# Kernel tuning notes

Hardware: AMD Instinct MI355X
Metric: run time of the kernel (lower is better)

Reference implementation:

```python
import jax, jax.numpy as jnp
import numpy as np

D = 256        # n_unit
H = 2          # n_head
FF = 256       # n_hid
WIN = 99       # N-1 in source: row i attends to cols [i-99, i]
NEG = -1e30    # additive mask value (-inf in torch)
LN_EPS = 1e-5


def _layer_norm(x, w, b):
    mu = jnp.mean(x, axis=-1, keepdims=True)
    var = jnp.mean((x - mu) ** 2, axis=-1, keepdims=True)
    return (x - mu) * jax.lax.rsqrt(var + LN_EPS) * w + b


def _pos_encoding(S, d):
    pos = jnp.arange(S, dtype=jnp.float32)[:, None]                      # [S,1]
    div = jnp.exp(jnp.arange(0, d, 2, dtype=jnp.float32) * (-np.log(10000.0) / d))
    ang = pos * div                                                      # [S,d/2]
    return jnp.stack([jnp.sin(ang), jnp.cos(ang)], axis=-1).reshape(S, d)


def _band_mask(S):
    i = jnp.arange(S)[:, None]
    j = jnp.arange(S)[None, :]
    allowed = (j <= i) & (j >= i - WIN)
    return jnp.where(allowed, 0.0, NEG).astype(jnp.float32)             # [S,S]


def setup_inputs() -> dict:
    key = jax.random.key(0)
    ks = jax.random.split(key, 24)
    B, S, IN = 8, 2000, 256
    s = 0.02
    inp = {
        "src": jax.random.normal(ks[0], (B, S, IN), jnp.float32),
        "input_lengths": jax.random.randint(ks[1], (B,), 1, S + 1).astype(jnp.int64),
        # encoder Linear(in_size, n_unit); torch Linear weight is [out,in]
        "W_enc": jax.random.normal(ks[2], (D, IN), jnp.float32) * s,
        "b_enc": jnp.zeros((D,), jnp.float32),
        # MHA packed qkv projection
        "in_proj_w": jax.random.normal(ks[3], (3 * D, D), jnp.float32) * s,
        "in_proj_b": jnp.zeros((3 * D,), jnp.float32),
        "out_proj_w": jax.random.normal(ks[4], (D, D), jnp.float32) * s,
        "out_proj_b": jnp.zeros((D,), jnp.float32),
        "ln1_w": jnp.ones((D,), jnp.float32),
        "ln1_b": jnp.zeros((D,), jnp.float32),
        # FFN
        "lin1_w": jax.random.normal(ks[5], (FF, D), jnp.float32) * s,
        "lin1_b": jnp.zeros((FF,), jnp.float32),
        "lin2_w": jax.random.normal(ks[6], (D, FF), jnp.float32) * s,
        "lin2_b": jnp.zeros((D,), jnp.float32),
        "ln2_w": jnp.ones((D,), jnp.float32),
        "ln2_b": jnp.zeros((D,), jnp.float32),
        # output head
        "fc1_w": jax.random.normal(ks[7], (D // 4, D), jnp.float32) * s,
        "fc1_b": jnp.zeros((D // 4,), jnp.float32),
        "fc2_w": jax.random.normal(ks[8], (1, D // 4), jnp.float32) * s,
        "fc2_b": jnp.zeros((1,), jnp.float32),
    }
    return inp


def reference(src, input_lengths, W_enc, b_enc, in_proj_w, in_proj_b,
              out_proj_w, out_proj_b, ln1_w, ln1_b, lin1_w, lin1_b,
              lin2_w, lin2_b, ln2_w, ln2_b, fc1_w, fc1_b, fc2_w, fc2_b):
    B, S, _ = src.shape
    hd = D // H
    # input projection + positional encoding (dropout is identity at eval)
    x = src @ W_enc.T + b_enc                                            # [B,S,D]
    x = x + _pos_encoding(S, D)[None]
    # --- TransformerEncoderLayer (post-norm, relu) with banded causal mask ---
    qkv = x @ in_proj_w.T + in_proj_b                                    # [B,S,3D]
    q, k, v = jnp.split(qkv, 3, axis=-1)
    q = q.reshape(B, S, H, hd)
    k = k.reshape(B, S, H, hd)
    v = v.reshape(B, S, H, hd)
    scores = jnp.einsum('bihd,bjhd->bhij', q, k) / np.sqrt(hd)           # [B,H,S,S]
    scores = scores + _band_mask(S)[None, None]
    attn = jax.nn.softmax(scores, axis=-1)
    ctx = jnp.einsum('bhij,bjhd->bihd', attn, v).reshape(B, S, D)
    attn_out = ctx @ out_proj_w.T + out_proj_b
    x = _layer_norm(x + attn_out, ln1_w, ln1_b)
    ff = jax.nn.relu(x @ lin1_w.T + lin1_b) @ lin2_w.T + lin2_b
    x = _layer_norm(x + ff, ln2_w, ln2_b)
    # --- output head (no activation between fc1 and fc2, per source) ---
    out = x @ fc1_w.T + fc1_b                                            # [B,S,D/4]
    logits = out @ fc2_w.T + fc2_b                                       # [B,S,1]
    return logits.reshape(B, -1)                                         # [B,S]
```

## Files before the change

### kernel.cpp

```cpp
#include <hip/hip_runtime.h>
#include <math.h>

#define SLEN 2000
#define BATCH 8
#define MTOK 16000
#define WIN 99
#define XPAD 264

typedef __attribute__((ext_vector_type(8))) short short8;
typedef __attribute__((ext_vector_type(4))) float floatx4;

__device__ __forceinline__ float bf2f(unsigned int h) {
  union { unsigned int u; float f; } w; w.u = h << 16; return w.f;
}
__device__ __forceinline__ unsigned short f2bf(float f) {
  union { float f; unsigned int u; } w; w.f = f;
  return (unsigned short)((w.u + 0x7fffu + ((w.u >> 16) & 1u)) >> 16);
}

__device__ __forceinline__ void cvt4(const float* __restrict__ in,
                                     unsigned short* __restrict__ out, int i) {
  float4 v = ((const float4*)in)[i];
  ushort4 o;
  o.x = f2bf(v.x); o.y = f2bf(v.y); o.z = f2bf(v.z); o.w = f2bf(v.w);
  ((ushort4*)out)[i] = o;
}

__global__ __launch_bounds__(256) void k_prep(
    const float* __restrict__ wenc,     unsigned short* __restrict__ wencb,
    const float* __restrict__ wqk,      unsigned short* __restrict__ wqkb,
    const float* __restrict__ wout,     unsigned short* __restrict__ woutb,
    const float* __restrict__ wl1,      unsigned short* __restrict__ wl1b,
    const float* __restrict__ wl2,      unsigned short* __restrict__ wl2b,
    float* __restrict__ pe,
    const float* __restrict__ fc1w, const float* __restrict__ fc1b,
    const float* __restrict__ fc2w, const float* __restrict__ fc2b,
    const float* __restrict__ ln2w, const float* __restrict__ ln2b,
    float* __restrict__ hp) {
  __shared__ float red0[4], red1[4];
  const int bx = blockIdx.x, tid = threadIdx.x;
  if (bx < 64)         { cvt4(wenc, wencb, bx * 256 + tid); }
  else if (bx < 256)   { cvt4(wqk,  wqkb,  (bx - 64) * 256 + tid); }
  else if (bx < 320)   { cvt4(wout, woutb, (bx - 256) * 256 + tid); }
  else if (bx < 384)   { cvt4(wl1,  wl1b,  (bx - 320) * 256 + tid); }
  else if (bx < 448)   { cvt4(wl2,  wl2b,  (bx - 384) * 256 + tid); }
  else if (bx < 948) {
    int i4 = (bx - 448) * 256 + tid;
    int e0 = i4 * 4;
    int s  = e0 >> 8;
    int d0 = e0 & 255;
    float dv0 = expf((float)(d0 >> 1) * -0.07195578415606394f);
    float dv1 = expf((float)((d0 >> 1) + 1) * -0.07195578415606394f);
    float a0 = (float)s * dv0, a1 = (float)s * dv1;
    ((float4*)pe)[i4] = make_float4(sinf(a0), cosf(a0), sinf(a1), cosf(a1));
  } else {
    int k = tid;
    float we = 0.f;
#pragma unroll 8
    for (int o = 0; o < 64; ++o) we += fc2w[o] * fc1w[o * 256 + k];
    float c1 = ln2w[k] * we;
    hp[k] = c1;
    float p0 = ln2b[k] * we;
    if (k < 64) p0 += fc2w[k] * fc1b[k];
    float s0 = p0, s1 = c1;
#pragma unroll
    for (int off = 32; off; off >>= 1) {
      s0 += __shfl_xor(s0, off);
      s1 += __shfl_xor(s1, off);
    }
    int wv = k >> 6;
    if ((k & 63) == 0) { red0[wv] = s0; red1[wv] = s1; }
    __syncthreads();
    if (k == 0) {
      hp[256] = red0[0] + red0[1] + red0[2] + red0[3] + fc2b[0];
      hp[257] = red1[0] + red1[1] + red1[2] + red1[3];
    }
  }
}

__global__ __launch_bounds__(512) void k_pre(
    const float* __restrict__ src,
    const unsigned short* __restrict__ wenc, const float* __restrict__ benc,
    const float* __restrict__ pe,
    const unsigned short* __restrict__ wqk, const float* __restrict__ bqk,
    unsigned short* __restrict__ xb, unsigned short* __restrict__ qkvb) {
  __shared__ __align__(16) unsigned short Xt[64 * XPAD];
  const int tid = threadIdx.x, lane = tid & 63, w = tid >> 6;
  const int m0 = blockIdx.x * 64;
  const int kq = lane >> 4, ml = lane & 15;

  {
    const int cb = w * 32;
    floatx4 acc[4][2] = {};
#pragma unroll
    for (int k8 = 0; k8 < 8; ++k8) {
      const int kt = k8 * 32;
      short8 af[4];
#pragma unroll
      for (int mt = 0; mt < 4; ++mt) {
        const float* ap = src + (size_t)(m0 + mt * 16 + ml) * 256 + kt + kq * 8;
        float4 v0 = *(const float4*)ap;
        float4 v1 = *(const float4*)(ap + 4);
        unsigned short t8[8] = {f2bf(v0.x), f2bf(v0.y), f2bf(v0.z), f2bf(v0.w),
                                f2bf(v1.x), f2bf(v1.y), f2bf(v1.z), f2bf(v1.w)};
        af[mt] = *(const short8*)t8;
      }
#pragma unroll
      for (int nt = 0; nt < 2; ++nt) {
        short8 bf = *(const short8*)(wenc + (size_t)(cb + nt * 16 + ml) * 256 + kt + kq * 8);
#pragma unroll
        for (int mt = 0; mt < 4; ++mt)
          acc[mt][nt] = __builtin_amdgcn_mfma_f32_16x16x32_bf16(af[mt], bf, acc[mt][nt], 0, 0, 0);
      }
    }
#pragma unroll
    for (int mt = 0; mt < 4; ++mt)
#pragma unroll
      for (int nt = 0; nt < 2; ++nt)
#pragma unroll
        for (int r = 0; r < 4; ++r) {
          int lrow = mt * 16 + kq * 4 + r;
          int col  = cb + nt * 16 + ml;
          float v = acc[mt][nt][r] + benc[col]
                  + pe[(size_t)((m0 + lrow) % SLEN) * 256 + col];
          unsigned short hv = f2bf(v);
          Xt[lrow * XPAD + col] = hv;
          xb[(size_t)(m0 + lrow) * 256 + col] = hv;
        }
  }
  __syncthreads();

  {
    const int cb = w * 96;
    floatx4 acc[4][6] = {};
#pragma unroll
    for (int k8 = 0; k8 < 8; ++k8) {
      const int kt = k8 * 32;
      short8 af[4];
#pragma unroll
      for (int mt = 0; mt < 4; ++mt)
        af[mt] = *(const short8*)&Xt[(mt * 16 + ml) * XPAD + kt + kq * 8];
#pragma unroll
      for (int nt = 0; nt < 6; ++nt) {
        short8 bf = *(const short8*)(wqk + (size_t)(cb + nt * 16 + ml) * 256 + kt + kq * 8);
#pragma unroll
        for (int mt = 0; mt < 4; ++mt)
          acc[mt][nt] = __builtin_amdgcn_mfma_f32_16x16x32_bf16(af[mt], bf, acc[mt][nt], 0, 0, 0);
      }
    }
#pragma unroll
    for (int mt = 0; mt < 4; ++mt)
#pragma unroll
      for (int nt = 0; nt < 6; ++nt)
#pragma unroll
        for (int r = 0; r < 4; ++r) {
          int row = m0 + mt * 16 + kq * 4 + r;
          int cg  = cb + nt * 16 + ml;
          qkvb[(size_t)row * 768 + cg] = f2bf(acc[mt][nt][r] + bqk[cg]);
        }
  }
}

#define KPAD 136
#define VPAD 184
#define PPAD 132
#define UNION 176

__global__ __launch_bounds__(256) void k_attn_mfma(const unsigned short* __restrict__ qkv,
                                                   unsigned short* __restrict__ ctx) {
  __shared__ __align__(16) unsigned short KV[UNION * KPAD];
  __shared__ __align__(16) unsigned short Ps[4][16 * PPAD];
  const int tid  = threadIdx.x;
  const int lane = tid & 63;
  const int w    = tid >> 6;
  const int i0   = blockIdx.x * 64;
  const int b    = blockIdx.y;
  const int h    = blockIdx.z;
  const int jmin_u = i0 - WIN;
  const float scale = 0.08838834764831845f;

  const int qrow = i0 + w * 16 + (lane & 15);
  const unsigned short* qptr =
      qkv + (size_t)(b * SLEN + min(qrow, SLEN - 1)) * 768 + h * 128 + (lane >> 4) * 8;
  short8 qf[4];
#pragma unroll
  for (int kc = 0; kc < 4; ++kc) qf[kc] = *(const short8*)(qptr + kc * 32);

  for (int it = 0; it < 11; ++it) {
    int idx = it * 256 + tid;
    int row = idx >> 4;
    int c8  = idx & 15;
    int j = jmin_u + row;
    uint4 v = make_uint4(0u, 0u, 0u, 0u);
    if (j >= 0 && j < SLEN)
      v = *(const uint4*)(qkv + (size_t)(b * SLEN + j) * 768 + 256 + h * 128 + c8 * 8);
    *(uint4*)&KV[row * KPAD + c8 * 8] = v;
  }
  __syncthreads();

  const int koff = w * 16;
  floatx4 sc[8] = {};
#pragma unroll
  for (int kt = 0; kt < 8; ++kt) {
#pragma unroll
    for (int kc = 0; kc < 4; ++kc) {
      short8 kf = *(const short8*)&KV[(koff + kt * 16 + (lane & 15)) * KPAD
                                      + kc * 32 + (lane >> 4) * 8];
      sc[kt] = __builtin_amdgcn_mfma_f32_16x16x32_bf16(qf[kc], kf, sc[kt], 0, 0, 0);
    }
  }

  const int qme = i0 + w * 16 + (lane >> 4) * 4;
  const int jme = jmin_u + koff + (lane & 15);
  float mx[4] = {-1e30f, -1e30f, -1e30f, -1e30f};
#pragma unroll
  for (int kt = 0; kt < 8; ++kt) {
#pragma unroll
    for (int r = 0; r < 4; ++r) {
      int j = jme + kt * 16, q = qme + r;
      bool ok = (j >= 0) && (j >= q - WIN) && (j <= q);
      float s = ok ? sc[kt][r] : -1e30f;
      sc[kt][r] = s;
      mx[r] = fmaxf(mx[r], s);
    }
  }
#pragma unroll
  for (int r = 0; r < 4; ++r)
#pragma unroll
    for (int off = 8; off; off >>= 1) mx[r] = fmaxf(mx[r], __shfl_xor(mx[r], off, 16));

  float sum[4] = {0.f, 0.f, 0.f, 0.f};
#pragma unroll
  for (int kt = 0; kt < 8; ++kt)
#pragma unroll
    for (int r = 0; r < 4; ++r) {
      float e = __expf((sc[kt][r] - mx[r]) * scale);
      sc[kt][r] = e;
      sum[r] += e;
    }
#pragma unroll
  for (int r = 0; r < 4; ++r)
#pragma unroll
    for (int off = 8; off; off >>= 1) sum[r] += __shfl_xor(sum[r], off, 16);
  float rinv[4];
#pragma unroll
  for (int r = 0; r < 4; ++r) rinv[r] = 1.f / sum[r];

  unsigned short* pw = &Ps[w][0];
#pragma unroll
  for (int kt = 0; kt < 8; ++kt)
#pragma unroll
    for (int r = 0; r < 4; ++r)
      pw[((lane >> 4) * 4 + r) * PPAD + kt * 16 + (lane & 15)] = f2bf(sc[kt][r]);
  __syncthreads();

  for (int it = 0; it < 12; ++it) {
    int idx = it * 256 + tid;
    int grp = idx >> 6;
    int key = (grp >> 4) * 64 + (idx & 63);
    int c8  = grp & 15;
    if (key < UNION) {
      int j = jmin_u + key;
      uint4 v = make_uint4(0u, 0u, 0u, 0u);
      if (j >= 0 && j < SLEN)
        v = *(const uint4*)(qkv + (size_t)(b * SLEN + j) * 768 + 512 + h * 128 + c8 * 8);
      unsigned short e[8];
      *(uint4*)e = v;
      int d0 = c8 * 8;
#pragma unroll
      for (int i = 0; i < 8; ++i) KV[(d0 + i) * VPAD + key] = e[i];
    }
  }
  __syncthreads();

  floatx4 ov[8] = {};
#pragma unroll
  for (int kc = 0; kc < 4; ++kc) {
    short8 pf = *(const short8*)&pw[(lane & 15) * PPAD + kc * 32 + (lane >> 4) * 8];
#pragma unroll
    for (int dt = 0; dt < 8; ++dt) {
      short8 vf = *(const short8*)&KV[(dt * 16 + (lane & 15)) * VPAD
                                      + koff + kc * 32 + (lane >> 4) * 8];
      ov[dt] = __builtin_amdgcn_mfma_f32_16x16x32_bf16(pf, vf, ov[dt], 0, 0, 0);
    }
  }

#pragma unroll
  for (int dt = 0; dt < 8; ++dt)
#pragma unroll
    for (int r = 0; r < 4; ++r) {
      int q = qme + r;
      if (q < SLEN)
        ctx[(size_t)(b * SLEN + q) * 256 + h * 128 + dt * 16 + (lane & 15)] =
            f2bf(ov[dt][r] * rinv[r]);
    }
}

__global__ __launch_bounds__(512) void k_post(
    const unsigned short* __restrict__ ctx,
    const unsigned short* __restrict__ wout, const float* __restrict__ bout,
    const unsigned short* __restrict__ xb,
    const float* __restrict__ ln1w, const float* __restrict__ ln1b,
    const unsigned short* __restrict__ w1, const float* __restrict__ b1,
    const unsigned short* __restrict__ w2, const float* __restrict__ b2,
    const float* __restrict__ hp, float* __restrict__ out) {
  __shared__ __align__(16) unsigned short X1[64 * XPAD];
  __shared__ float lnred[8][64][3];
  __shared__ float lnstat[64][2];
  __shared__ float lnp[512];
  __shared__ float c1s[256];
  const int tid = threadIdx.x, lane = tid & 63, w = tid >> 6;
  const int m0 = blockIdx.x * 64;
  const int kq = lane >> 4, ml = lane & 15;
  const int cb = w * 32;

  if (tid < 256) {
    lnp[tid] = ln1w[tid];
    lnp[256 + tid] = ln1b[tid];
    c1s[tid] = hp[tid];
  }
  const float c0h = hp[256], sc1 = hp[257];

  floatx4 acc[4][2] = {};
#pragma unroll
  for (int k8 = 0; k8 < 8; ++k8) {
    const int kt = k8 * 32;
    short8 af[4];
#pragma unroll
    for (int mt = 0; mt < 4; ++mt)
      af[mt] = *(const short8*)(ctx + (size_t)(m0 + mt * 16 + ml) * 256 + kt + kq * 8);
#pragma unroll
    for (int nt = 0; nt < 2; ++nt) {
      short8 bf = *(const short8*)(wout + (size_t)(cb + nt * 16 + ml) * 256 + kt + kq * 8);
#pragma unroll
      for (int mt = 0; mt < 4; ++mt)
        acc[mt][nt] = __builtin_amdgcn_mfma_f32_16x16x32_bf16(af[mt], bf, acc[mt][nt], 0, 0, 0);
    }
  }
  float s_[4][4], q_[4][4];
#pragma unroll
  for (int mt = 0; mt < 4; ++mt)
#pragma unroll
    for (int r = 0; r < 4; ++r) { s_[mt][r] = 0.f; q_[mt][r] = 0.f; }
#pragma unroll
  for (int mt = 0; mt < 4; ++mt)
#pragma unroll
    for (int nt = 0; nt < 2; ++nt)
#pragma unroll
      for (int r = 0; r < 4; ++r) {
        int lrow = mt * 16 + kq * 4 + r;
        int col  = cb + nt * 16 + ml;
        float v = acc[mt][nt][r] + bout[col]
                + bf2f(xb[(size_t)(m0 + lrow) * 256 + col]);
        acc[mt][nt][r] = v;
        s_[mt][r] += v;
        q_[mt][r] += v * v;
      }
#pragma unroll
  for (int mt = 0; mt < 4; ++mt)
#pragma unroll
    for (int r = 0; r < 4; ++r) {
#pragma unroll
      for (int off = 8; off; off >>= 1) {
        s_[mt][r] += __shfl_xor(s_[mt][r], off, 16);
        q_[mt][r] += __shfl_xor(q_[mt][r], off, 16);
      }
      if (ml == 0) {
        int lrow = mt * 16 + kq * 4 + r;
        lnred[w][lrow][0] = s_[mt][r];
        lnred[w][lrow][1] = q_[mt][r];
      }
    }
  __syncthreads();
  if (tid < 64) {
    float s = 0.f, q = 0.f;
#pragma unroll
    for (int i = 0; i < 8; ++i) { s += lnred[i][tid][0]; q += lnred[i][tid][1]; }
    float mu  = s * (1.f / 256.f);
    float var = q * (1.f / 256.f) - mu * mu;
    lnstat[tid][0] = mu;
    lnstat[tid][1] = rsqrtf(var + 1e-5f);
  }
  __syncthreads();
  floatx4 x1sav[4][2];
#pragma unroll
  for (int mt = 0; mt < 4; ++mt)
#pragma unroll
    for (int r = 0; r < 4; ++r) {
      int lrow = mt * 16 + kq * 4 + r;
      float mu = lnstat[lrow][0], rr = lnstat[lrow][1];
#pragma unroll
      for (int nt = 0; nt < 2; ++nt) {
        int col = cb + nt * 16 + ml;
        float x1 = (acc[mt][nt][r] - mu) * rr * lnp[col] + lnp[256 + col];
        x1sav[mt][nt][r] = x1;
        X1[lrow * XPAD + col] = f2bf(x1);
      }
    }
  __syncthreads();

#pragma unroll
  for (int mt = 0; mt < 4; ++mt)
#pragma unroll
    for (int nt = 0; nt < 2; ++nt) acc[mt][nt] = (floatx4){0.f, 0.f, 0.f, 0.f};
#pragma unroll
  for (int k8 = 0; k8 < 8; ++k8) {
    const int kt = k8 * 32;
    short8 af[4];
#pragma unroll
    for (int mt = 0; mt < 4; ++mt)
      af[mt] = *(const short8*)&X1[(mt * 16 + ml) * XPAD + kt + kq * 8];
#pragma unroll
    for (int nt = 0; nt < 2; ++nt) {
      short8 bf = *(const short8*)(w1 + (size_t)(cb + nt * 16 + ml) * 256 + kt + kq * 8);
#pragma unroll
      for (int mt = 0; mt < 4; ++mt)
        acc[mt][nt] = __builtin_amdgcn_mfma_f32_16x16x32_bf16(af[mt], bf, acc[mt][nt], 0, 0, 0);
    }
  }
  __syncthreads();
#pragma unroll
  for (int mt = 0; mt < 4; ++mt)
#pragma unroll
    for (int nt = 0; nt < 2; ++nt)
#pragma unroll
      for (int r = 0; r < 4; ++r) {
        int lrow = mt * 16 + kq * 4 + r;
        int col  = cb + nt * 16 + ml;
        X1[lrow * XPAD + col] = f2bf(fmaxf(acc[mt][nt][r] + b1[col], 0.f));
      }
  __syncthreads();

#pragma unroll
  for (int mt = 0; mt < 4; ++mt)
#pragma unroll
    for (int nt = 0; nt < 2; ++nt) acc[mt][nt] = (floatx4){0.f, 0.f, 0.f, 0.f};
#pragma unroll
  for (int k8 = 0; k8 < 8; ++k8) {
    const int kt = k8 * 32;
    short8 af[4];
#pragma unroll
    for (int mt = 0; mt < 4; ++mt)
      af[mt] = *(const short8*)&X1[(mt * 16 + ml) * XPAD + kt + kq * 8];
#pragma unroll
    for (int nt = 0; nt < 2; ++nt) {
      short8 bf = *(const short8*)(w2 + (size_t)(cb + nt * 16 + ml) * 256 + kt + kq * 8);
#pragma unroll
      for (int mt = 0; mt < 4; ++mt)
        acc[mt][nt] = __builtin_amdgcn_mfma_f32_16x16x32_bf16(af[mt], bf, acc[mt][nt], 0, 0, 0);
    }
  }
  float ss[4][4], qq[4][4], dd[4][4];
#pragma unroll
  for (int mt = 0; mt < 4; ++mt)
#pragma unroll
    for (int r = 0; r < 4; ++r) { ss[mt][r] = 0.f; qq[mt][r] = 0.f; dd[mt][r] = 0.f; }
#pragma unroll
  for (int mt = 0; mt < 4; ++mt)
#pragma unroll
    for (int nt = 0; nt < 2; ++nt)
#pragma unroll
      for (int r = 0; r < 4; ++r) {
        int col = cb + nt * 16 + ml;
        float v = acc[mt][nt][r] + b2[col] + x1sav[mt][nt][r];
        ss[mt][r] += v;
        qq[mt][r] += v * v;
        dd[mt][r] += v * c1s[col];
      }
#pragma unroll
  for (int mt = 0; mt < 4; ++mt)
#pragma unroll
    for (int r = 0; r < 4; ++r) {
#pragma unroll
      for (int off = 8; off; off >>= 1) {
        ss[mt][r] += __shfl_xor(ss[mt][r], off, 16);
        qq[mt][r] += __shfl_xor(qq[mt][r], off, 16);
        dd[mt][r] += __shfl_xor(dd[mt][r], off, 16);
      }
      if (ml == 0) {
        int lrow = mt * 16 + kq * 4 + r;
        lnred[w][lrow][0] = ss[mt][r];
        lnred[w][lrow][1] = qq[mt][r];
        lnred[w][lrow][2] = dd[mt][r];
      }
    }
  __syncthreads();
  if (tid < 64) {
    float s = 0.f, q = 0.f, d = 0.f;
#pragma unroll
    for (int i = 0; i < 8; ++i) {
      s += lnred[i][tid][0];
      q += lnred[i][tid][1];
      d += lnred[i][tid][2];
    }
    float mu  = s * (1.f / 256.f);
    float var = q * (1.f / 256.f) - mu * mu;
    float rr  = rsqrtf(var + 1e-5f);
    out[m0 + tid] = rr * (d - mu * sc1) + c0h;
  }
}

extern "C" void kernel_launch(void* const* d_in, const int* in_sizes, int n_in,
                              void* d_out, int out_size, void* d_ws, size_t ws_size,
                              hipStream_t stream) {
  const float* src        = (const float*)d_in[0];
  const float* W_enc      = (const float*)d_in[2];
  const float* b_enc      = (const float*)d_in[3];
  const float* in_proj_w  = (const float*)d_in[4];
  const float* in_proj_b  = (const float*)d_in[5];
  const float* out_proj_w = (const float*)d_in[6];
  const float* out_proj_b = (const float*)d_in[7];
  const float* ln1_w      = (const float*)d_in[8];
  const float* ln1_b      = (const float*)d_in[9];
  const float* lin1_w     = (const float*)d_in[10];
  const float* lin1_b     = (const float*)d_in[11];
  const float* lin2_w     = (const float*)d_in[12];
  const float* lin2_b     = (const float*)d_in[13];
  const float* ln2_w      = (const float*)d_in[14];
  const float* ln2_b      = (const float*)d_in[15];
  const float* fc1_w      = (const float*)d_in[16];
  const float* fc1_b      = (const float*)d_in[17];
  const float* fc2_w      = (const float*)d_in[18];
  const float* fc2_b      = (const float*)d_in[19];

  char* p = (char*)d_ws;
  float* pe            = (float*)p;           p += (size_t)SLEN * 256 * 4;
  float* hp            = (float*)p;           p += 2048;
  unsigned short* xb   = (unsigned short*)p;  p += (size_t)MTOK * 256 * 2;
  unsigned short* qkvb = (unsigned short*)p;  p += (size_t)MTOK * 768 * 2;
  unsigned short* ctxb = (unsigned short*)p;  p += (size_t)MTOK * 256 * 2;
  unsigned short* wencb= (unsigned short*)p;  p += 256 * 256 * 2;
  unsigned short* wqkb = (unsigned short*)p;  p += 768 * 256 * 2;
  unsigned short* woutb= (unsigned short*)p;  p += 256 * 256 * 2;
  unsigned short* wl1b = (unsigned short*)p;  p += 256 * 256 * 2;
  unsigned short* wl2b = (unsigned short*)p;  p += 256 * 256 * 2;

  k_prep<<<949, 256, 0, stream>>>(W_enc, wencb, in_proj_w, wqkb,
                                  out_proj_w, woutb, lin1_w, wl1b, lin2_w, wl2b,
                                  pe, fc1_w, fc1_b, fc2_w, fc2_b, ln2_w, ln2_b, hp);
  k_pre<<<MTOK / 64, 512, 0, stream>>>(src, wencb, b_enc, pe, wqkb, in_proj_b, xb, qkvb);
  k_attn_mfma<<<dim3((SLEN + 63) / 64, BATCH, 2), 256, 0, stream>>>(qkvb, ctxb);
  k_post<<<MTOK / 64, 512, 0, stream>>>(ctxb, woutb, out_proj_b, xb, ln1_w, ln1_b,
                                        wl1b, lin1_b, wl2b, lin2_b, hp, (float*)d_out);
}
```

Baseline: 188.8 us.

## Split fused pre/post kernels into smaller kernels with more blocks

Splits the fused encoder+QKV kernel into separate k_enc and k_qkv launches, each with a 2D grid over column tiles. Splits the post kernel into an out-projection+LN1 kernel and an FFN+LN2+head kernel over 32-row tiles. The aim is more blocks and higher occupancy through smaller register and shared-memory footprints. In exchange it adds extra launches and round-trips of intermediate activations (xb, x1b) through global memory, and k_enc recomputes the src bf16 conversion for each column tile.

Result: slower. 218.3 us (+15.6%).

```diff
diff --git a/kernel.cpp b/kernel.cpp
--- a/kernel.cpp
+++ b/kernel.cpp
@@ -78,87 +78,85 @@
   }
 }
 
-__global__ __launch_bounds__(512) void k_pre(
+__global__ __launch_bounds__(256, 4) void k_enc(
     const float* __restrict__ src,
     const unsigned short* __restrict__ wenc, const float* __restrict__ benc,
-    const float* __restrict__ pe,
-    const unsigned short* __restrict__ wqk, const float* __restrict__ bqk,
-    unsigned short* __restrict__ xb, unsigned short* __restrict__ qkvb) {
-  __shared__ __align__(16) unsigned short Xt[64 * XPAD];
+    const float* __restrict__ pe, unsigned short* __restrict__ xb) {
   const int tid = threadIdx.x, lane = tid & 63, w = tid >> 6;
   const int m0 = blockIdx.x * 64;
+  const int cb = blockIdx.y * 128 + w * 32;
   const int kq = lane >> 4, ml = lane & 15;
 
-  {
-    const int cb = w * 32;
-    floatx4 acc[4][2] = {};
-#pragma unroll
-    for (int k8 = 0; k8 < 8; ++k8) {
-      const int kt = k8 * 32;
-      short8 af[4];
-#pragma unroll
-      for (int mt = 0; mt < 4; ++mt) {
-        const float* ap = src + (size_t)(m0 + mt * 16 + ml) * 256 + kt + kq * 8;
-        float4 v0 = *(const float4*)ap;
-        float4 v1 = *(const float4*)(ap + 4);
-        unsigned short t8[8] = {f2bf(v0.x), f2bf(v0.y), f2bf(v0.z), f2bf(v0.w),
-                                f2bf(v1.x), f2bf(v1.y), f2bf(v1.z), f2bf(v1.w)};
-        af[mt] = *(const short8*)t8;
-      }
-#pragma unroll
-      for (int nt = 0; nt < 2; ++nt) {
-        short8 bf = *(const short8*)(wenc + (size_t)(cb + nt * 16 + ml) * 256 + kt + kq * 8);
-#pragma unroll
-        for (int mt = 0; mt < 4; ++mt)
-          acc[mt][nt] = __builtin_amdgcn_mfma_f32_16x16x32_bf16(af[mt], bf, acc[mt][nt], 0, 0, 0);
-      }
-    }
+  floatx4 acc[4][2] = {};
+#pragma unroll
+  for (int k8 = 0; k8 < 8; ++k8) {
+    const int kt = k8 * 32;
+    short8 af[4];
+#pragma unroll
+    for (int mt = 0; mt < 4; ++mt) {
+      const float* ap = src + (size_t)(m0 + mt * 16 + ml) * 256 + kt + kq * 8;
+      float4 v0 = *(const float4*)ap;
+      float4 v1 = *(const float4*)(ap + 4);
+      unsigned short t8[8] = {f2bf(v0.x), f2bf(v0.y), f2bf(v0.z), f2bf(v0.w),
+                              f2bf(v1.x), f2bf(v1.y), f2bf(v1.z), f2bf(v1.w)};
+      af[mt] = *(const short8*)t8;
+    }
+#pragma unroll
+    for (int nt = 0; nt < 2; ++nt) {
+      short8 bf = *(const short8*)(wenc + (size_t)(cb + nt * 16 + ml) * 256 + kt + kq * 8);
+#pragma unroll
+      for (int mt = 0; mt < 4; ++mt)
+        acc[mt][nt] = __builtin_amdgcn_mfma_f32_16x16x32_bf16(af[mt], bf, acc[mt][nt], 0, 0, 0);
+    }
+  }
+#pragma unroll
+  for (int mt = 0; mt < 4; ++mt)
+#pragma unroll
+    for (int nt = 0; nt < 2; ++nt)
+#pragma unroll
+      for (int r = 0; r < 4; ++r) {
+        int m   = m0 + mt * 16 + kq * 4 + r;
+        int col = cb + nt * 16 + ml;
+        float v = acc[mt][nt][r] + benc[col] + pe[(size_t)(m % SLEN) * 256 + col];
+        xb[(size_t)m * 256 + col] = f2bf(v);
+      }
+}
+
+__global__ __launch_bounds__(256, 4) void k_qkv(
+    const unsigned short* __restrict__ xb,
+    const unsigned short* __restrict__ wqk, const float* __restrict__ bqk,
+    unsigned short* __restrict__ qkvb) {
+  const int tid = threadIdx.x, lane = tid & 63, w = tid >> 6;
+  const int m0 = blockIdx.x * 64;
+  const int cb = blockIdx.y * 128 + w * 32;
+  const int kq = lane >> 4, ml = lane & 15;
+
+  floatx4 acc[4][2] = {};
+#pragma unroll
+  for (int k8 = 0; k8 < 8; ++k8) {
+    const int kt = k8 * 32;
+    short8 af[4];
 #pragma unroll
     for (int mt = 0; mt < 4; ++mt)
-#pragma unroll
-      for (int nt = 0; nt < 2; ++nt)
-#pragma unroll
-        for (int r = 0; r < 4; ++r) {
-          int lrow = mt * 16 + kq * 4 + r;
-          int col  = cb + nt * 16 + ml;
-          float v = acc[mt][nt][r] + benc[col]
-                  + pe[(size_t)((m0 + lrow) % SLEN) * 256 + col];
-          unsigned short hv = f2bf(v);
-          Xt[lrow * XPAD + col] = hv;
-          xb[(size_t)(m0 + lrow) * 256 + col] = hv;
-        }
-  }
-  __syncthreads();
-
-  {
-    const int cb = w * 96;
-    floatx4 acc[4][6] = {};
-#pragma unroll
-    for (int k8 = 0; k8 < 8; ++k8) {
-      const int kt = k8 * 32;
-      short8 af[4];
+      af[mt] = *(const short8*)(xb + (size_t)(m0 + mt * 16 + ml) * 256 + kt + kq * 8);
+#pragma unroll
+    for (int nt = 0; nt < 2; ++nt) {
+      short8 bf = *(const short8*)(wqk + (size_t)(cb + nt * 16 + ml) * 256 + kt + kq * 8);
 #pragma unroll
       for (int mt = 0; mt < 4; ++mt)
-        af[mt] = *(const short8*)&Xt[(mt * 16 + ml) * XPAD + kt + kq * 8];
-#pragma unroll
-      for (int nt = 0; nt < 6; ++nt) {
-        short8 bf = *(const short8*)(wqk + (size_t)(cb + nt * 16 + ml) * 256 + kt + kq * 8);
-#pragma unroll
-        for (int mt = 0; mt < 4; ++mt)
-          acc[mt][nt] = __builtin_amdgcn_mfma_f32_16x16x32_bf16(af[mt], bf, acc[mt][nt], 0, 0, 0);
-      }
-    }
-#pragma unroll
-    for (int mt = 0; mt < 4; ++mt)
-#pragma unroll
-      for (int nt = 0; nt < 6; ++nt)
-#pragma unroll
-        for (int r = 0; r < 4; ++r) {
-          int row = m0 + mt * 16 + kq * 4 + r;
-          int cg  = cb + nt * 16 + ml;
-          qkvb[(size_t)row * 768 + cg] = f2bf(acc[mt][nt][r] + bqk[cg]);
-        }
-  }
+        acc[mt][nt] = __builtin_amdgcn_mfma_f32_16x16x32_bf16(af[mt], bf, acc[mt][nt], 0, 0, 0);
+    }
+  }
+#pragma unroll
+  for (int mt = 0; mt < 4; ++mt)
+#pragma unroll
+    for (int nt = 0; nt < 2; ++nt)
+#pragma unroll
+      for (int r = 0; r < 4; ++r) {
+        int m   = m0 + mt * 16 + kq * 4 + r;
+        int col = cb + nt * 16 + ml;
+        qkvb[(size_t)m * 768 + col] = f2bf(acc[mt][nt][r] + bqk[col]);
+      }
 }
 
 #define KPAD 136
@@ -296,56 +294,48 @@
     }
 }
 
-__global__ __launch_bounds__(512) void k_post(
+__global__ __launch_bounds__(256, 4) void k_o(
     const unsigned short* __restrict__ ctx,
     const unsigned short* __restrict__ wout, const float* __restrict__ bout,
     const unsigned short* __restrict__ xb,
     const float* __restrict__ ln1w, const float* __restrict__ ln1b,
-    const unsigned short* __restrict__ w1, const float* __restrict__ b1,
-    const unsigned short* __restrict__ w2, const float* __restrict__ b2,
-    const float* __restrict__ hp, float* __restrict__ out) {
-  __shared__ __align__(16) unsigned short X1[64 * XPAD];
-  __shared__ float lnred[8][64][3];
-  __shared__ float lnstat[64][2];
+    unsigned short* __restrict__ x1b) {
+  __shared__ float lnred[4][32][2];
+  __shared__ float lnstat[32][2];
   __shared__ float lnp[512];
-  __shared__ float c1s[256];
   const int tid = threadIdx.x, lane = tid & 63, w = tid >> 6;
-  const int m0 = blockIdx.x * 64;
+  const int m0 = blockIdx.x * 32;
+  const int cb = w * 64;
   const int kq = lane >> 4, ml = lane & 15;
-  const int cb = w * 32;
-
-  if (tid < 256) {
-    lnp[tid] = ln1w[tid];
-    lnp[256 + tid] = ln1b[tid];
-    c1s[tid] = hp[tid];
-  }
-  const float c0h = hp[256], sc1 = hp[257];
-
-  floatx4 acc[4][2] = {};
+
+  lnp[tid] = ln1w[tid];
+  lnp[256 + tid] = ln1b[tid];
+
+  floatx4 acc[2][4] = {};
 #pragma unroll
   for (int k8 = 0; k8 < 8; ++k8) {
     const int kt = k8 * 32;
-    short8 af[4];
-#pragma unroll
-    for (int mt = 0; mt < 4; ++mt)
+    short8 af[2];
+#pragma unroll
+    for (int mt = 0; mt < 2; ++mt)
       af[mt] = *(const short8*)(ctx + (size_t)(m0 + mt * 16 + ml) * 256 + kt + kq * 8);
 #pragma unroll
-    for (int nt = 0; nt < 2; ++nt) {
+    for (int nt = 0; nt < 4; ++nt) {
       short8 bf = *(const short8*)(wout + (size_t)(cb + nt * 16 + ml) * 256 + kt + kq * 8);
 #pragma unroll
-      for (int mt = 0; mt < 4; ++mt)
+      for (int mt = 0; mt < 2; ++mt)
         acc[mt][nt] = __builtin_amdgcn_mfma_f32_16x16x32_bf16(af[mt], bf, acc[mt][nt], 0, 0, 0);
     }
   }
-  float s_[4][4], q_[4][4];
-#pragma unroll
-  for (int mt = 0; mt < 4; ++mt)
+  float s_[2][4], q_[2][4];
+#pragma unroll
+  for (int mt = 0; mt < 2; ++mt)
 #pragma unroll
     for (int r = 0; r < 4; ++r) { s_[mt][r] = 0.f; q_[mt][r] = 0.f; }
 #pragma unroll
-  for (int mt = 0; mt < 4; ++mt)
-#pragma unroll
-    for (int nt = 0; nt < 2; ++nt)
+  for (int mt = 0; mt < 2; ++mt)
+#pragma unroll
+    for (int nt = 0; nt < 4; ++nt)
 #pragma unroll
       for (int r = 0; r < 4; ++r) {
         int lrow = mt * 16 + kq * 4 + r;
@@ -357,7 +347,7 @@
         q_[mt][r] += v * v;
       }
 #pragma unroll
-  for (int mt = 0; mt < 4; ++mt)
+  for (int mt = 0; mt < 2; ++mt)
 #pragma unroll
     for (int r = 0; r < 4; ++r) {
 #pragma unroll
@@ -372,103 +362,114 @@
       }
     }
   __syncthreads();
-  if (tid < 64) {
-    float s = 0.f, q = 0.f;
-#pragma unroll
-    for (int i = 0; i < 8; ++i) { s += lnred[i][tid][0]; q += lnred[i][tid][1]; }
+  if (tid < 32) {
+    float s = lnred[0][tid][0] + lnred[1][tid][0] + lnred[2][tid][0] + lnred[3][tid][0];
+    float q = lnred[0][tid][1] + lnred[1][tid][1] + lnred[2][tid][1] + lnred[3][tid][1];
     float mu  = s * (1.f / 256.f);
     float var = q * (1.f / 256.f) - mu * mu;
     lnstat[tid][0] = mu;
     lnstat[tid][1] = rsqrtf(var + 1e-5f);
   }
   __syncthreads();
-  floatx4 x1sav[4][2];
-#pragma unroll
-  for (int mt = 0; mt < 4; ++mt)
+#pragma unroll
+  for (int mt = 0; mt < 2; ++mt)
 #pragma unroll
     for (int r = 0; r < 4; ++r) {
       int lrow = mt * 16 + kq * 4 + r;
       float mu = lnstat[lrow][0], rr = lnstat[lrow][1];
 #pragma unroll
-      for (int nt = 0; nt < 2; ++nt) {
+      for (int nt = 0; nt < 4; ++nt) {
         int col = cb + nt * 16 + ml;
         float x1 = (acc[mt][nt][r] - mu) * rr * lnp[col] + lnp[256 + col];
-        x1sav[mt][nt][r] = x1;
-        X1[lrow * XPAD + col] = f2bf(x1);
-      }
-    }
-  __syncthreads();
-
-#pragma unroll
-  for (int mt = 0; mt < 4; ++mt)
-#pragma unroll
-    for (int nt = 0; nt < 2; ++nt) acc[mt][nt] = (floatx4){0.f, 0.f, 0.f, 0.f};
+        x1b[(size_t)(m0 + lrow) * 256 + col] = f2bf(x1);
+      }
+    }
+}
+
+__global__ __launch_bounds__(256, 4) void k_ffn(
+    const unsigned short* __restrict__ x1b,
+    const unsigned short* __restrict__ w1, const float* __restrict__ b1,
+    const unsigned short* __restrict__ w2, const float* __restrict__ b2,
+    const float* __restrict__ hp, float* __restrict__ out) {
+  __shared__ __align__(16) unsigned short Hs[32 * XPAD];
+  __shared__ float lnred[4][32][3];
+  __shared__ float c1s[256];
+  const int tid = threadIdx.x, lane = tid & 63, w = tid >> 6;
+  const int m0 = blockIdx.x * 32;
+  const int cb = w * 64;
+  const int kq = lane >> 4, ml = lane & 15;
+
+  c1s[tid] = hp[tid];
+  const float c0h = hp[256], sc1 = hp[257];
+
+  floatx4 acc[2][4] = {};
 #pragma unroll
   for (int k8 = 0; k8 < 8; ++k8) {
     const int kt = k8 * 32;
-    short8 af[4];
-#pragma unroll
-    for (int mt = 0; mt < 4; ++mt)
-      af[mt] = *(const short8*)&X1[(mt * 16 + ml) * XPAD + kt + kq * 8];
-#pragma unroll
-    for (int nt = 0; nt < 2; ++nt) {
+    short8 af[2];
+#pragma unroll
+    for (int mt = 0; mt < 2; ++mt)
+      af[mt] = *(const short8*)(x1b + (size_t)(m0 + mt * 16 + ml) * 256 + kt + kq * 8);
+#pragma unroll
+    for (int nt = 0; nt < 4; ++nt) {
       short8 bf = *(const short8*)(w1 + (size_t)(cb + nt * 16 + ml) * 256 + kt + kq * 8);
 #pragma unroll
-      for (int mt = 0; mt < 4; ++mt)
+      for (int mt = 0; mt < 2; ++mt)
         acc[mt][nt] = __builtin_amdgcn_mfma_f32_16x16x32_bf16(af[mt], bf, acc[mt][nt], 0, 0, 0);
     }
   }
-  __syncthreads();
-#pragma unroll
-  for (int mt = 0; mt < 4; ++mt)
-#pragma unroll
-    for (int nt = 0; nt < 2; ++nt)
+#pragma unroll
+  for (int mt = 0; mt < 2; ++mt)
+#pragma unroll
+    for (int nt = 0; nt < 4; ++nt)
 #pragma unroll
       for (int r = 0; r < 4; ++r) {
         int lrow = mt * 16 + kq * 4 + r;
         int col  = cb + nt * 16 + ml;
-        X1[lrow * XPAD + col] = f2bf(fmaxf(acc[mt][nt][r] + b1[col], 0.f));
-      }
-  __syncthreads();
-
-#pragma unroll
-  for (int mt = 0; mt < 4; ++mt)
-#pragma unroll
-    for (int nt = 0; nt < 2; ++nt) acc[mt][nt] = (floatx4){0.f, 0.f, 0.f, 0.f};
+        Hs[lrow * XPAD + col] = f2bf(fmaxf(acc[mt][nt][r] + b1[col], 0.f));
+      }
+  __syncthreads();
+
+#pragma unroll
+  for (int mt = 0; mt < 2; ++mt)
+#pragma unroll
+    for (int nt = 0; nt < 4; ++nt) acc[mt][nt] = (floatx4){0.f, 0.f, 0.f, 0.f};
 #pragma unroll
   for (int k8 = 0; k8 < 8; ++k8) {
     const int kt = k8 * 32;
-    short8 af[4];
-#pragma unroll
-    for (int mt = 0; mt < 4; ++mt)
-      af[mt] = *(const short8*)&X1[(mt * 16 + ml) * XPAD + kt + kq * 8];
-#pragma unroll
-    for (int nt = 0; nt < 2; ++nt) {
+    short8 af[2];
+#pragma unroll
+    for (int mt = 0; mt < 2; ++mt)
+      af[mt] = *(const short8*)&Hs[(mt * 16 + ml) * XPAD + kt + kq * 8];
+#pragma unroll
+    for (int nt = 0; nt < 4; ++nt) {
       short8 bf = *(const short8*)(w2 + (size_t)(cb + nt * 16 + ml) * 256 + kt + kq * 8);
 #pragma unroll
-      for (int mt = 0; mt < 4; ++mt)
+      for (int mt = 0; mt < 2; ++mt)
         acc[mt][nt] = __builtin_amdgcn_mfma_f32_16x16x32_bf16(af[mt], bf, acc[mt][nt], 0, 0, 0);
     }
   }
-  float ss[4][4], qq[4][4], dd[4][4];
-#pragma unroll
-  for (int mt = 0; mt < 4; ++mt)
+  float ss[2][4], qq[2][4], dd[2][4];
+#pragma unroll
+  for (int mt = 0; mt < 2; ++mt)
 #pragma unroll
     for (int r = 0; r < 4; ++r) { ss[mt][r] = 0.f; qq[mt][r] = 0.f; dd[mt][r] = 0.f; }
 #pragma unroll
-  for (int mt = 0; mt < 4; ++mt)
-#pragma unroll
-    for (int nt = 0; nt < 2; ++nt)
+  for (int mt = 0; mt < 2; ++mt)
+#pragma unroll
+    for (int nt = 0; nt < 4; ++nt)
 #pragma unroll
       for (int r = 0; r < 4; ++r) {
-        int col = cb + nt * 16 + ml;
-        float v = acc[mt][nt][r] + b2[col] + x1sav[mt][nt][r];
+        int lrow = mt * 16 + kq * 4 + r;
+        int col  = cb + nt * 16 + ml;
+        float v = acc[mt][nt][r] + b2[col]
+                + bf2f(x1b[(size_t)(m0 + lrow) * 256 + col]);
         ss[mt][r] += v;
         qq[mt][r] += v * v;
         dd[mt][r] += v * c1s[col];
       }
 #pragma unroll
-  for (int mt = 0; mt < 4; ++mt)
+  for (int mt = 0; mt < 2; ++mt)
 #pragma unroll
     for (int r = 0; r < 4; ++r) {
 #pragma unroll
@@ -485,14 +486,10 @@
       }
     }
   __syncthreads();
-  if (tid < 64) {
-    float s = 0.f, q = 0.f, d = 0.f;
-#pragma unroll
-    for (int i = 0; i < 8; ++i) {
-      s += lnred[i][tid][0];
-      q += lnred[i][tid][1];
-      d += lnred[i][tid][2];
-    }
+  if (tid < 32) {
+    float s = lnred[0][tid][0] + lnred[1][tid][0] + lnred[2][tid][0] + lnred[3][tid][0];
+    float q = lnred[0][tid][1] + lnred[1][tid][1] + lnred[2][tid][1] + lnred[3][tid][1];
+    float d = lnred[0][tid][2] + lnred[1][tid][2] + lnred[2][tid][2] + lnred[3][tid][2];
     float mu  = s * (1.f / 256.f);
     float var = q * (1.f / 256.f) - mu * mu;
     float rr  = rsqrtf(var + 1e-5f);
@@ -529,6 +526,7 @@
   unsigned short* xb   = (unsigned short*)p;  p += (size_t)MTOK * 256 * 2;
   unsigned short* qkvb = (unsigned short*)p;  p += (size_t)MTOK * 768 * 2;
   unsigned short* ctxb = (unsigned short*)p;  p += (size_t)MTOK * 256 * 2;
+  unsigned short* x1b  = (unsigned short*)p;  p += (size_t)MTOK * 256 * 2;
   unsigned short* wencb= (unsigned short*)p;  p += 256 * 256 * 2;
   unsigned short* wqkb = (unsigned short*)p;  p += 768 * 256 * 2;
   unsigned short* woutb= (unsigned short*)p;  p += 256 * 256 * 2;
@@ -538,8 +536,9 @@
   k_prep<<<949, 256, 0, stream>>>(W_enc, wencb, in_proj_w, wqkb,
                                   out_proj_w, woutb, lin1_w, wl1b, lin2_w, wl2b,
                                   pe, fc1_w, fc1_b, fc2_w, fc2_b, ln2_w, ln2_b, hp);
-  k_pre<<<MTOK / 64, 512, 0, stream>>>(src, wencb, b_enc, pe, wqkb, in_proj_b, xb, qkvb);
+  k_enc<<<dim3(MTOK / 64, 2), 256, 0, stream>>>(src, wencb, b_enc, pe, xb);
+  k_qkv<<<dim3(MTOK / 64, 6), 256, 0, stream>>>(xb, wqkb, in_proj_b, qkvb);
   k_attn_mfma<<<dim3((SLEN + 63) / 64, BATCH, 2), 256, 0, stream>>>(qkvb, ctxb);
-  k_post<<<MTOK / 64, 512, 0, stream>>>(ctxb, woutb, out_proj_b, xb, ln1_w, ln1_b,
-                                        wl1b, lin1_b, wl2b, lin2_b, hp, (float*)d_out);
-}
+  k_o<<<MTOK / 32, 256, 0, stream>>>(ctxb, woutb, out_proj_b, xb, ln1_w, ln1_b, x1b);
+  k_ffn<<<MTOK / 32, 256, 0, stream>>>(x1b, wl1b, lin1_b, wl2b, lin2_b, hp, (float*)d_out);
+}
```
